# Kernel tuning notes

Hardware: AMD Instinct MI355X
Metric: run time of the kernel (lower is better)

## Reference

```python
import jax, jax.numpy as jnp
import numpy as np

C = 256; G = 16; GC = C // G; K = 3; P = K * K
N = 4; H = 64; W = 64
PAD = 1; OFFSET_SCALE = 1.0; LN_EPS = 1e-5


def setup_inputs() -> dict:
    key = jax.random.key(0)
    ks = jax.random.split(key, 8)
    s = 0.02
    return {
        "x": jax.random.normal(ks[0], (N, C, H, W), jnp.float32),
        "dw_w": jax.random.normal(ks[1], (C, 1, K, K), jnp.float32) * s,
        "dw_b": jnp.zeros((C,), jnp.float32),
        "ln_g": jnp.ones((C,), jnp.float32),
        "ln_b": jnp.zeros((C,), jnp.float32),
        "off_w": jax.random.normal(ks[2], (C, G * P * 2), jnp.float32) * s,
        "off_b": jnp.zeros((G * P * 2,), jnp.float32),
        "mask_w": jax.random.normal(ks[3], (C, G * P), jnp.float32) * s,
        "mask_b": jnp.zeros((G * P,), jnp.float32),
        "inp_w": jax.random.normal(ks[4], (C, C), jnp.float32) * s,
        "inp_b": jnp.zeros((C,), jnp.float32),
        "out_w": jax.random.normal(ks[5], (C, C), jnp.float32) * s,
        "out_b": jnp.zeros((C,), jnp.float32),
    }


def _dcnv3_nchw(x, dw_w, dw_b, ln_g, ln_b, off_w, off_b, mask_w, mask_b,
                inp_w, inp_b, out_w, out_b):
    # NCHW -> NHWC (wrapper permute)
    xn = jnp.transpose(x, (0, 2, 3, 1))                      # (N,H,W,C)
    x_proj = xn @ inp_w + inp_b                              # input_proj

    # offset/mask branch: depthwise conv (NCHW) -> LayerNorm (channels-last) -> GELU
    x1 = jax.lax.conv_general_dilated(
        x, dw_w, window_strides=(1, 1), padding=((PAD, PAD), (PAD, PAD)),
        dimension_numbers=("NCHW", "OIHW", "NCHW"), feature_group_count=C)
    x1 = jnp.transpose(x1, (0, 2, 3, 1)) + dw_b
    mu = x1.mean(-1, keepdims=True)
    var = ((x1 - mu) ** 2).mean(-1, keepdims=True)
    x1 = (x1 - mu) * jax.lax.rsqrt(var + LN_EPS) * ln_g + ln_b
    x1 = jax.nn.gelu(x1, approximate=False)

    offset = (x1 @ off_w + off_b).reshape(N, H, W, G, P, 2)  # (x,y) pairs
    mask = jax.nn.softmax((x1 @ mask_w + mask_b).reshape(N, H, W, G, P), axis=-1)

    # pad sampled feature map with zeros (F.pad before sampling)
    xp = jnp.pad(x_proj, ((0, 0), (PAD, PAD), (PAD, PAD), (0, 0)))
    Hin, Win = H + 2 * PAD, W + 2 * PAD
    xg = xp.reshape(N, Hin, Win, G, GC)

    # reference points, normalized by padded size
    ref_y = (jnp.arange(H, dtype=jnp.float32) + PAD + 0.5) / Hin
    ref_x = (jnp.arange(W, dtype=jnp.float32) + PAD + 0.5) / Win
    ref = jnp.stack([jnp.broadcast_to(ref_x[None, :], (H, W)),
                     jnp.broadcast_to(ref_y[:, None], (H, W))], -1)  # (H,W,2)

    # dilation grid: x varies in the outer loop (torch meshgrid 'ij')
    d = jnp.arange(K, dtype=jnp.float32) - (K - 1) // 2     # [-1,0,1]
    gx = jnp.repeat(d, K) / Win
    gy = jnp.tile(d, K) / Hin
    grid = jnp.stack([gx, gy], -1)                           # (P,2)

    norm = jnp.array([Win, Hin], jnp.float32)
    loc = (ref[None, :, :, None, None, :] + grid * OFFSET_SCALE
           + offset * OFFSET_SCALE / norm)                   # (N,H,W,G,P,2)

    # grid_sample bilinear, align_corners=False, zero padding
    px = loc[..., 0] * Win - 0.5
    py = loc[..., 1] * Hin - 0.5
    x0 = jnp.floor(px); y0 = jnp.floor(py)
    wx = px - x0; wy = py - y0
    x0i = x0.astype(jnp.int32); y0i = y0.astype(jnp.int32)

    n_idx = jnp.arange(N)[:, None, None, None, None]
    g_idx = jnp.arange(G)[None, None, None, :, None]

    def corner(iy, ix, w):
        valid = (iy >= 0) & (iy < Hin) & (ix >= 0) & (ix < Win)
        v = xg[n_idx, jnp.clip(iy, 0, Hin - 1), jnp.clip(ix, 0, Win - 1), g_idx]
        wgt = jnp.where(valid, w, 0.0) * mask                # fold mask into weights
        return jnp.einsum("nhwgp,nhwgpc->nhwgc", wgt, v)

    out = (corner(y0i, x0i, (1 - wy) * (1 - wx))
           + corner(y0i, x0i + 1, (1 - wy) * wx)
           + corner(y0i + 1, x0i, wy * (1 - wx))
           + corner(y0i + 1, x0i + 1, wy * wx))               # (N,H,W,G,GC)

    out = out.reshape(N, H, W, C) @ out_w + out_b            # output_proj
    return jnp.transpose(out, (0, 3, 1, 2))                  # NHWC -> NCHW


def reference(x, dw_w, dw_b, ln_g, ln_b, off_w, off_b, mask_w, mask_b,
              inp_w, inp_b, out_w, out_b):
    return _dcnv3_nchw(x, dw_w, dw_b, ln_g, ln_b, off_w, off_b,
                       mask_w, mask_b, inp_w, inp_b, out_w, out_b)
```

## Files before the change

### kernel.cpp

```cpp
#include <hip/hip_runtime.h>
#include <hip/hip_bf16.h>
#include <math.h>


using bf16x8 = __attribute__((ext_vector_type(8))) short;
using f32x4  = __attribute__((ext_vector_type(4))) float;

#define GLOBAL_AS __attribute__((address_space(1)))
#define LDS_AS    __attribute__((address_space(3)))

static __device__ inline void g2lds16(const void* g, void* l) {
  __builtin_amdgcn_global_load_lds((const GLOBAL_AS int*)g, (LDS_AS int*)l, 16, 0, 0);
}
static __device__ inline unsigned short f2bf(float v) {
  __hip_bfloat16 b = __float2bfloat16(v);
  return *reinterpret_cast<unsigned short*>(&b);
}
static __device__ inline float us2f(unsigned short u) {
  union { unsigned u; float f; } c; c.u = ((unsigned)u) << 16; return c.f;
}

__global__ __launch_bounds__(256) void prep_w_k(
    const float* __restrict__ inp_w, const float* __restrict__ off_w,
    const float* __restrict__ off_b, const float* __restrict__ mask_w,
    const float* __restrict__ mask_b, const float* __restrict__ out_w,
    __hip_bfloat16* __restrict__ BtI, __hip_bfloat16* __restrict__ BtOM,
    __hip_bfloat16* __restrict__ BtO, float* __restrict__ bOM)
{
  const int b = blockIdx.x, t = threadIdx.x;
  if (b < 256) {
    int n = b;
    BtI[n * 256 + t] = __float2bfloat16(inp_w[t * 256 + n]);
  } else if (b < 768) {
    int n = b - 256;
    float v = 0.f;
    if (n < 288) v = off_w[t * 288 + n];
    else if (n < 432) v = mask_w[t * 144 + (n - 288)];
    BtOM[n * 256 + t] = __float2bfloat16(v);
    if (b == 256) {
      for (int idx = t; idx < 512; idx += 256) {
        float bv = (idx < 288) ? off_b[idx] : ((idx < 432) ? mask_b[idx - 288] : 0.f);
        bOM[idx] = bv;
      }
    }
  } else {
    int n = b - 768;
    BtO[n * 256 + t] = __float2bfloat16(out_w[t * 256 + n]);
  }
}

__global__ __launch_bounds__(1024) void stage2_gi_k(
    const float* __restrict__ x,
    const float* __restrict__ dw_w, const float* __restrict__ dw_b,
    const float* __restrict__ ln_g, const float* __restrict__ ln_b,
    const __hip_bfloat16* __restrict__ BtOM, const float* __restrict__ bOM,
    __hip_bfloat16* __restrict__ om,
    const __hip_bfloat16* __restrict__ BtI, const float* __restrict__ inp_b,
    __hip_bfloat16* __restrict__ xpu)
{
  __shared__ __align__(16) char smem[57344];
  const int bid = blockIdx.x;
  const int t = threadIdx.x;

  if (bid >= 256) {
    unsigned short* A = (unsigned short*)smem;
    float* ftile = (float*)(smem + 33792);

    const int strip = bid - 256;
    const int n4 = strip >> 6, hw0 = (strip & 63) * 64;
    const float* xb = x + (size_t)n4 * 1048576 + hw0;

    const int cl0 = t >> 6, wl0 = t & 63;
    const int cl1 = (t + 1024) >> 6, wl1 = (t + 1024) & 63;
    float p0 = xb[(size_t)cl0 * 4096 + wl0];
    float p1 = xb[(size_t)cl1 * 4096 + wl1];

    for (int ck = 0; ck < 8; ++ck) {
      const int ch0 = ck * 32;
      ftile[cl0 * 65 + wl0] = p0;
      ftile[cl1 * 65 + wl1] = p1;
      if (ck < 7) {
        p0 = xb[(size_t)(ch0 + 32 + cl0) * 4096 + wl0];
        p1 = xb[(size_t)(ch0 + 32 + cl1) * 4096 + wl1];
      }
      __syncthreads();
      {
        int px = t >> 4, cq2 = t & 15;
        unsigned short b0 = f2bf(ftile[(cq2 * 2) * 65 + px]);
        unsigned short b1 = f2bf(ftile[(cq2 * 2 + 1) * 65 + px]);
        *(unsigned*)&A[px * 264 + ch0 + cq2 * 2] =
            (unsigned)b0 | ((unsigned)b1 << 16);
      }
      __syncthreads();
    }

    const int wave = t >> 6, lane = t & 63;
    const int quad = lane >> 4, lr = lane & 15;
    const int wm = wave >> 2, wn = wave & 3;

    bf16x8 areg[8];
    #pragma unroll
    for (int s = 0; s < 8; ++s)
      areg[s] = *(const bf16x8*)&A[(wm * 16 + lr) * 264 + s * 32 + quad * 8];
    __syncthreads();

    auto stageI = [&](int s, int buf) {
      int col = t >> 2, kq = t & 3;
      g2lds16(BtI + (size_t)col * 256 + s * 32 + kq * 8,
              smem + buf * 16384 + t * 16);
    };

    f32x4 acc[4];
    #pragma unroll
    for (int i = 0; i < 4; ++i) acc[i] = (f32x4){0.f, 0.f, 0.f, 0.f};

    stageI(0, 0);
    __syncthreads();
    #pragma unroll
    for (int s = 0; s < 8; ++s) {
      if (s < 7) stageI(s + 1, (s + 1) & 1);
      const short* B = (const short*)(smem + (s & 1) * 16384);
      bf16x8 bfr[4];
      #pragma unroll
      for (int ni = 0; ni < 4; ++ni)
        bfr[ni] = *(const bf16x8*)&B[(wn * 64 + ni * 16 + lr) * 32 + quad * 8];
      #pragma unroll
      for (int ni = 0; ni < 4; ++ni)
        acc[ni] = __builtin_amdgcn_mfma_f32_16x16x32_bf16(areg[s], bfr[ni], acc[ni], 0, 0, 0);
      __syncthreads();
    }

    const size_t m0 = (size_t)strip * 64;
    #pragma unroll
    for (int ni = 0; ni < 4; ++ni) {
      int col = wn * 64 + ni * 16 + lr;
      float bv = inp_b[col];
      #pragma unroll
      for (int reg = 0; reg < 4; ++reg) {
        size_t m = m0 + wm * 16 + quad * 4 + reg;
        xpu[m * 256 + col] = __float2bfloat16(acc[ni][reg] + bv);
      }
    }
    return;
  }

  unsigned short* x1t = (unsigned short*)smem;
  float* psq  = (float*)(smem + 33792);
  float* murs = (float*)(smem + 41984);

  const int blk = ((bid & 7) << 5) | (bid >> 3);
  const int n4 = blk >> 6, h = blk & 63;
  const int w = t & 63, q = t >> 6;

  const float* xb = x + (size_t)n4 * 1048576;
  const bool hm = (h > 0), hp = (h < 63);
  float av[16];
  float s1 = 0.f, s2 = 0.f;

  #pragma unroll 2
  for (int j = 0; j < 8; ++j) {
    #pragma unroll
    for (int u = 0; u < 2; ++u) {
      const int c = q * 16 + 2 * j + u;
      const float* xc = xb + (size_t)c * 4096 + h * 64 + w;
      float v0 = hm ? xc[-64] : 0.f;
      float v1 = xc[0];
      float v2 = hp ? xc[64] : 0.f;
      const float* wp = dw_w + c * 9;
      float a = dw_b[c];
      #pragma unroll
      for (int dh = 0; dh < 3; ++dh) {
        float v = (dh == 0) ? v0 : (dh == 1) ? v1 : v2;
        float vm = __shfl(v, w - 1, 64);
        float vp = __shfl(v, w + 1, 64);
        if (w == 0)  vm = 0.f;
        if (w == 63) vp = 0.f;
        a = fmaf(vm, wp[dh * 3 + 0], a);
        a = fmaf(v,  wp[dh * 3 + 1], a);
        a = fmaf(vp, wp[dh * 3 + 2], a);
      }
      s1 += a;
      s2 = fmaf(a, a, s2);
      av[2 * j + u] = a;
    }
  }

  psq[q * 64 + w] = s1;
  psq[1024 + q * 64 + w] = s2;
  __syncthreads();
  if (t < 64) {
    float a = 0.f, b = 0.f;
    #pragma unroll
    for (int j = 0; j < 16; ++j) { a += psq[j * 64 + t]; b += psq[1024 + j * 64 + t]; }
    float mu = a * (1.f / 256.f);
    murs[t] = mu;
    murs[64 + t] = rsqrtf(b * (1.f / 256.f) - mu * mu + 1e-5f);
  }
  __syncthreads();
  {
    float mu = murs[w], rs = murs[64 + w];
    #pragma unroll
    for (int j = 0; j < 8; ++j) {
      int c = q * 16 + 2 * j;
      float y0 = fmaf((av[2 * j] - mu) * rs, ln_g[c], ln_b[c]);
      float y1 = fmaf((av[2 * j + 1] - mu) * rs, ln_g[c + 1], ln_b[c + 1]);
      float g0 = 0.5f * y0 * (1.f + erff(y0 * 0.70710678f));
      float g1 = 0.5f * y1 * (1.f + erff(y1 * 0.70710678f));
      *(unsigned*)&x1t[w * 264 + c] = (unsigned)f2bf(g0) | ((unsigned)f2bf(g1) << 16);
    }
  }
  __syncthreads();

  const int wave = t >> 6, lane = t & 63;
  const int quad = lane >> 4, lr = lane & 15;
  const int wm = wave >> 2, wn = wave & 3;

  bf16x8 areg[8];
  #pragma unroll
  for (int s = 0; s < 8; ++s)
    areg[s] = *(const bf16x8*)&x1t[(wm * 16 + lr) * 264 + s * 32 + quad * 8];
  __syncthreads();

  auto stageOM = [&](int s, int buf) {
    char* dst = smem + buf * 28672;
    int col = t >> 2, kq = t & 3;
    g2lds16(BtOM + (size_t)col * 256 + s * 32 + kq * 8, dst + t * 16);
    int jj = t + 1024;
    if (jj < 1792) {
      int col2 = jj >> 2, kq2 = jj & 3;
      g2lds16(BtOM + (size_t)col2 * 256 + s * 32 + kq2 * 8, dst + jj * 16);
    }
  };

  f32x4 acc[7];
  #pragma unroll
  for (int i = 0; i < 7; ++i) acc[i] = (f32x4){0.f, 0.f, 0.f, 0.f};

  stageOM(0, 0);
  __syncthreads();
  #pragma unroll
  for (int s = 0; s < 8; ++s) {
    if (s < 7) stageOM(s + 1, (s + 1) & 1);
    const short* B = (const short*)(smem + (s & 1) * 28672);
    bf16x8 bfr[7];
    #pragma unroll
    for (int ni = 0; ni < 7; ++ni)
      bfr[ni] = *(const bf16x8*)&B[(wn * 112 + ni * 16 + lr) * 32 + quad * 8];
    #pragma unroll
    for (int ni = 0; ni < 7; ++ni)
      acc[ni] = __builtin_amdgcn_mfma_f32_16x16x32_bf16(areg[s], bfr[ni], acc[ni], 0, 0, 0);
    __syncthreads();
  }

  const size_t pix0 = (size_t)n4 * 4096 + (size_t)h * 64;
  #pragma unroll
  for (int ni = 0; ni < 7; ++ni) {
    int col = wn * 112 + ni * 16 + lr;
    if (col < 432) {
      float bv = bOM[col];
      #pragma unroll
      for (int reg = 0; reg < 4; ++reg) {
        int m = wm * 16 + quad * 4 + reg;
        om[(pix0 + m) * 448 + col] = __float2bfloat16(acc[ni][reg] + bv);
      }
    }
  }
}

__global__ __launch_bounds__(512) void fused_so_k(
    const __hip_bfloat16* __restrict__ xpu, const __hip_bfloat16* __restrict__ om,
    const __hip_bfloat16* __restrict__ BtO, const float* __restrict__ out_b,
    float* __restrict__ out)
{
  __shared__ __align__(16) char smem[49664];
  unsigned short* st = (unsigned short*)smem;

  const int bid = blockIdx.x;
  const int swz = ((bid & 7) << 6) | (bid >> 3);
  const int pix0 = swz << 5;
  const int t = threadIdx.x;

  auto stageO = [&](int s, int buf) {
    char* dst = smem + 16896 + buf * 16384;
    #pragma unroll
    for (int r = 0; r < 2; ++r) {
      int j = t + r * 512;
      int col = j >> 2, kq = j & 3;
      g2lds16(BtO + (size_t)col * 256 + s * 32 + kq * 8, dst + j * 16);
    }
  };

  stageO(0, 0);

  {
    const int pl = t >> 4, g = t & 15;
    const int pix = pix0 + pl;
    const int n4s = pix >> 12;
    const int hw = pix & 4095;
    const int h = hw >> 6, w = hw & 63;
    const unsigned short* omp = (const unsigned short*)om + (size_t)pix * 448;

    float mk[9];
    {
      float mx = -1e30f;
      #pragma unroll
      for (int p = 0; p < 9; ++p) { mk[p] = us2f(omp[288 + g * 9 + p]); mx = fmaxf(mx, mk[p]); }
      float se = 0.f;
      #pragma unroll
      for (int p = 0; p < 9; ++p) { mk[p] = __expf(mk[p] - mx); se += mk[p]; }
      float inv = 1.f / se;
      #pragma unroll
      for (int p = 0; p < 9; ++p) mk[p] *= inv;
    }

    const __hip_bfloat16* xpg = xpu + (g << 4);
    float ax[16];
    #pragma unroll
    for (int i = 0; i < 16; ++i) ax[i] = 0.f;

    auto corner = [&](int iy, int ix, float wt) {
      if ((unsigned)(iy - 1) >= 64u || (unsigned)(ix - 1) >= 64u) return;
      const __hip_bfloat16* src =
          xpg + ((size_t)((n4s << 12) + (iy - 1) * 64 + (ix - 1)) << 8);
      uint4 u0 = *(const uint4*)src;
      uint4 u1 = *(const uint4*)(src + 8);
      const unsigned uu[8] = {u0.x, u0.y, u0.z, u0.w, u1.x, u1.y, u1.z, u1.w};
      #pragma unroll
      for (int i = 0; i < 8; ++i) {
        float lo = us2f((unsigned short)(uu[i] & 0xffff));
        float hi = us2f((unsigned short)(uu[i] >> 16));
        ax[2 * i + 0] = fmaf(wt, lo, ax[2 * i + 0]);
        ax[2 * i + 1] = fmaf(wt, hi, ax[2 * i + 1]);
      }
    };

    #pragma unroll
    for (int p = 0; p < 9; ++p) {
      float ox = us2f(omp[g * 18 + 2 * p]), oy = us2f(omp[g * 18 + 2 * p + 1]);
      float px = (float)(w + p / 3) + ox;
      float py = (float)(h + p % 3) + oy;
      float xf = floorf(px), yf = floorf(py);
      float wx = px - xf, wy = py - yf;
      int ix = (int)xf, iy = (int)yf;
      float m = mk[p];
      corner(iy,     ix,     (1.f - wy) * (1.f - wx) * m);
      corner(iy,     ix + 1, (1.f - wy) * wx * m);
      corner(iy + 1, ix,     wy * (1.f - wx) * m);
      corner(iy + 1, ix + 1, wy * wx * m);
    }

    unsigned short ub[16];
    #pragma unroll
    for (int i = 0; i < 16; ++i) ub[i] = f2bf(ax[i]);
    uint4 u0, u1;
    u0.x = (unsigned)ub[0] | ((unsigned)ub[1] << 16);
    u0.y = (unsigned)ub[2] | ((unsigned)ub[3] << 16);
    u0.z = (unsigned)ub[4] | ((unsigned)ub[5] << 16);
    u0.w = (unsigned)ub[6] | ((unsigned)ub[7] << 16);
    u1.x = (unsigned)ub[8] | ((unsigned)ub[9] << 16);
    u1.y = (unsigned)ub[10] | ((unsigned)ub[11] << 16);
    u1.z = (unsigned)ub[12] | ((unsigned)ub[13] << 16);
    u1.w = (unsigned)ub[14] | ((unsigned)ub[15] << 16);
    *(uint4*)&st[pl * 264 + g * 16] = u0;
    *(uint4*)&st[pl * 264 + g * 16 + 8] = u1;
  }
  __syncthreads();

  const int wave = t >> 6, lane = t & 63;
  const int quad = lane >> 4, lr = lane & 15;
  const int wm = wave >> 2, wn = wave & 3;

  bf16x8 areg[8];
  #pragma unroll
  for (int s = 0; s < 8; ++s)
    areg[s] = *(const bf16x8*)&st[(wm * 16 + lr) * 264 + s * 32 + quad * 8];

  f32x4 acc[4];
  #pragma unroll
  for (int i = 0; i < 4; ++i) acc[i] = (f32x4){0.f, 0.f, 0.f, 0.f};

  #pragma unroll
  for (int s = 0; s < 8; ++s) {
    if (s < 7) stageO(s + 1, (s + 1) & 1);
    const short* B = (const short*)(smem + 16896 + (s & 1) * 16384);
    bf16x8 bfr[4];
    #pragma unroll
    for (int ni = 0; ni < 4; ++ni)
      bfr[ni] = *(const bf16x8*)&B[(wn * 64 + ni * 16 + lr) * 32 + quad * 8];
    #pragma unroll
    for (int ni = 0; ni < 4; ++ni)
      acc[ni] = __builtin_amdgcn_mfma_f32_16x16x32_bf16(areg[s], bfr[ni], acc[ni], 0, 0, 0);
    __syncthreads();
  }

  const int n4 = pix0 >> 12, hw0 = pix0 & 4095;
  #pragma unroll
  for (int ni = 0; ni < 4; ++ni) {
    int col = wn * 64 + ni * 16 + lr;
    float bv = out_b[col];
    float4 v;
    v.x = acc[ni][0] + bv; v.y = acc[ni][1] + bv;
    v.z = acc[ni][2] + bv; v.w = acc[ni][3] + bv;
    *(float4*)&out[(size_t)(n4 * 256 + col) * 4096 + hw0 + wm * 16 + quad * 4] = v;
  }
}

extern "C" void kernel_launch(void* const* d_in, const int* in_sizes, int n_in,
                              void* d_out, int out_size, void* d_ws, size_t ws_size,
                              hipStream_t stream) {
  const float* x      = (const float*)d_in[0];
  const float* dw_w   = (const float*)d_in[1];
  const float* dw_b   = (const float*)d_in[2];
  const float* ln_g   = (const float*)d_in[3];
  const float* ln_b   = (const float*)d_in[4];
  const float* off_w  = (const float*)d_in[5];
  const float* off_b  = (const float*)d_in[6];
  const float* mask_w = (const float*)d_in[7];
  const float* mask_b = (const float*)d_in[8];
  const float* inp_w  = (const float*)d_in[9];
  const float* inp_b  = (const float*)d_in[10];
  const float* out_w  = (const float*)d_in[11];
  const float* out_b  = (const float*)d_in[12];
  float* out = (float*)d_out;

  char* w0 = (char*)d_ws;
  __hip_bfloat16* xpu  = (__hip_bfloat16*)(w0);
  __hip_bfloat16* om   = (__hip_bfloat16*)(w0 + 8388608);
  __hip_bfloat16* BtI  = (__hip_bfloat16*)(w0 + 23068672);
  __hip_bfloat16* BtOM = (__hip_bfloat16*)(w0 + 23199744);
  __hip_bfloat16* BtO  = (__hip_bfloat16*)(w0 + 23461888);
  float*          bOM  = (float*)(w0 + 23592960);
  if (ws_size < 23595008) return;

  prep_w_k<<<1024, 256, 0, stream>>>(inp_w, off_w, off_b, mask_w, mask_b,
                                     out_w, BtI, BtOM, BtO, bOM);
  stage2_gi_k<<<512, 1024, 0, stream>>>(x, dw_w, dw_b, ln_g, ln_b, BtOM, bOM,
                                        om, BtI, inp_b, xpu);
  fused_so_k<<<512, 512, 0, stream>>>(xpu, om, BtO, out_b, out);
}
```

Baseline: 152.2 us.

## Move offset/mask GEMM into sampling kernel, keep results in LDS

The offset/mask projection GEMM moves out of the depthwise/LayerNorm kernel, which now writes the GELU activations (256 bf16 per pixel) to global memory. The sampling kernel loads those activations, runs the 448-column GEMM per 32-pixel tile, and keeps the offsets and mask logits in LDS instead of reading them back from global. This drops the 448-wide om buffer round trip and shortens the first kernel, at the cost of more LDS per block (about 78 KB, which may reduce occupancy) and a longer sampling kernel.

```diff
diff --git a/kernel.cpp b/kernel.cpp
--- a/kernel.cpp
+++ b/kernel.cpp
@@ -53,12 +53,10 @@
     const float* __restrict__ x,
     const float* __restrict__ dw_w, const float* __restrict__ dw_b,
     const float* __restrict__ ln_g, const float* __restrict__ ln_b,
-    const __hip_bfloat16* __restrict__ BtOM, const float* __restrict__ bOM,
-    __hip_bfloat16* __restrict__ om,
     const __hip_bfloat16* __restrict__ BtI, const float* __restrict__ inp_b,
-    __hip_bfloat16* __restrict__ xpu)
+    __hip_bfloat16* __restrict__ xpu, __hip_bfloat16* __restrict__ x1g)
 {
-  __shared__ __align__(16) char smem[57344];
+  __shared__ __align__(16) char smem[42496];
   const int bid = blockIdx.x;
   const int t = threadIdx.x;
 
@@ -211,77 +209,51 @@
   }
   __syncthreads();
 
-  const int wave = t >> 6, lane = t & 63;
-  const int quad = lane >> 4, lr = lane & 15;
-  const int wm = wave >> 2, wn = wave & 3;
-
-  bf16x8 areg[8];
-  #pragma unroll
-  for (int s = 0; s < 8; ++s)
-    areg[s] = *(const bf16x8*)&x1t[(wm * 16 + lr) * 264 + s * 32 + quad * 8];
-  __syncthreads();
-
-  auto stageOM = [&](int s, int buf) {
-    char* dst = smem + buf * 28672;
-    int col = t >> 2, kq = t & 3;
-    g2lds16(BtOM + (size_t)col * 256 + s * 32 + kq * 8, dst + t * 16);
-    int jj = t + 1024;
-    if (jj < 1792) {
-      int col2 = jj >> 2, kq2 = jj & 3;
-      g2lds16(BtOM + (size_t)col2 * 256 + s * 32 + kq2 * 8, dst + jj * 16);
-    }
-  };
-
-  f32x4 acc[7];
-  #pragma unroll
-  for (int i = 0; i < 7; ++i) acc[i] = (f32x4){0.f, 0.f, 0.f, 0.f};
-
-  stageOM(0, 0);
-  __syncthreads();
-  #pragma unroll
-  for (int s = 0; s < 8; ++s) {
-    if (s < 7) stageOM(s + 1, (s + 1) & 1);
-    const short* B = (const short*)(smem + (s & 1) * 28672);
-    bf16x8 bfr[7];
-    #pragma unroll
-    for (int ni = 0; ni < 7; ++ni)
-      bfr[ni] = *(const bf16x8*)&B[(wn * 112 + ni * 16 + lr) * 32 + quad * 8];
-    #pragma unroll
-    for (int ni = 0; ni < 7; ++ni)
-      acc[ni] = __builtin_amdgcn_mfma_f32_16x16x32_bf16(areg[s], bfr[ni], acc[ni], 0, 0, 0);
-    __syncthreads();
-  }
-
   const size_t pix0 = (size_t)n4 * 4096 + (size_t)h * 64;
   #pragma unroll
-  for (int ni = 0; ni < 7; ++ni) {
-    int col = wn * 112 + ni * 16 + lr;
-    if (col < 432) {
-      float bv = bOM[col];
-      #pragma unroll
-      for (int reg = 0; reg < 4; ++reg) {
-        int m = wm * 16 + quad * 4 + reg;
-        om[(pix0 + m) * 448 + col] = __float2bfloat16(acc[ni][reg] + bv);
-      }
-    }
+  for (int r = 0; r < 2; ++r) {
+    int j = t + r * 1024;
+    int px = j >> 5, cu = j & 31;
+    *(uint4*)&x1g[(pix0 + px) * 256 + cu * 8] = *(const uint4*)&x1t[px * 264 + cu * 8];
   }
 }
 
 __global__ __launch_bounds__(512) void fused_so_k(
-    const __hip_bfloat16* __restrict__ xpu, const __hip_bfloat16* __restrict__ om,
+    const __hip_bfloat16* __restrict__ x1g, const __hip_bfloat16* __restrict__ xpu,
+    const __hip_bfloat16* __restrict__ BtOM, const float* __restrict__ bOM,
     const __hip_bfloat16* __restrict__ BtO, const float* __restrict__ out_b,
     float* __restrict__ out)
 {
-  __shared__ __align__(16) char smem[49664];
-  unsigned short* st = (unsigned short*)smem;
+  __shared__ __align__(16) char smem[78336];
+  unsigned short* x1s = (unsigned short*)smem;
+  unsigned short* st  = (unsigned short*)smem;
+  unsigned short* Som = (unsigned short*)(smem + 16896);
 
   const int bid = blockIdx.x;
   const int swz = ((bid & 7) << 6) | (bid >> 3);
   const int pix0 = swz << 5;
   const int t = threadIdx.x;
 
+  const int wave = t >> 6, lane = t & 63;
+  const int quad = lane >> 4, lr = lane & 15;
+  const int wm = wave >> 2, wn = wave & 3;
+
+  auto stageB = [&](int s, int buf) {
+    char* dst = smem + 16896 + buf * 28672;
+    #pragma unroll
+    for (int r = 0; r < 3; ++r) {
+      int j = t + r * 512;
+      int col = j >> 2, kq = j & 3;
+      g2lds16(BtOM + (size_t)col * 256 + s * 32 + kq * 8, dst + j * 16);
+    }
+    if (t < 256) {
+      int j = t + 1536;
+      int col = j >> 2, kq = j & 3;
+      g2lds16(BtOM + (size_t)col * 256 + s * 32 + kq * 8, dst + j * 16);
+    }
+  };
   auto stageO = [&](int s, int buf) {
-    char* dst = smem + 16896 + buf * 16384;
+    char* dst = smem + 45568 + buf * 16384;
     #pragma unroll
     for (int r = 0; r < 2; ++r) {
       int j = t + r * 512;
@@ -289,6 +261,50 @@
       g2lds16(BtO + (size_t)col * 256 + s * 32 + kq * 8, dst + j * 16);
     }
   };
+
+  #pragma unroll
+  for (int r = 0; r < 2; ++r) {
+    int j = t + r * 512;
+    int px = j >> 5, cu = j & 31;
+    g2lds16(x1g + (size_t)(pix0 + px) * 256 + cu * 8, smem + j * 16);
+  }
+  stageB(0, 0);
+  __syncthreads();
+
+  bf16x8 areg[8];
+  #pragma unroll
+  for (int s = 0; s < 8; ++s)
+    areg[s] = *(const bf16x8*)&x1s[(wm * 16 + lr) * 256 + s * 32 + quad * 8];
+
+  f32x4 acc[7];
+  #pragma unroll
+  for (int i = 0; i < 7; ++i) acc[i] = (f32x4){0.f, 0.f, 0.f, 0.f};
+
+  #pragma unroll
+  for (int s = 0; s < 8; ++s) {
+    if (s < 7) stageB(s + 1, (s + 1) & 1);
+    const short* B = (const short*)(smem + 16896 + (s & 1) * 28672);
+    bf16x8 bfr[7];
+    #pragma unroll
+    for (int ni = 0; ni < 7; ++ni)
+      bfr[ni] = *(const bf16x8*)&B[(wn * 112 + ni * 16 + lr) * 32 + quad * 8];
+    #pragma unroll
+    for (int ni = 0; ni < 7; ++ni)
+      acc[ni] = __builtin_amdgcn_mfma_f32_16x16x32_bf16(areg[s], bfr[ni], acc[ni], 0, 0, 0);
+    __syncthreads();
+  }
+
+  #pragma unroll
+  for (int ni = 0; ni < 7; ++ni) {
+    int col = wn * 112 + ni * 16 + lr;
+    float bv = bOM[col];
+    #pragma unroll
+    for (int reg = 0; reg < 4; ++reg) {
+      int m = wm * 16 + quad * 4 + reg;
+      Som[m * 448 + col] = f2bf(acc[ni][reg] + bv);
+    }
+  }
+  __syncthreads();
 
   stageO(0, 0);
 
@@ -298,7 +314,7 @@
     const int n4s = pix >> 12;
     const int hw = pix & 4095;
     const int h = hw >> 6, w = hw & 63;
-    const unsigned short* omp = (const unsigned short*)om + (size_t)pix * 448;
+    const unsigned short* omp = Som + pl * 448;
 
     float mk[9];
     {
@@ -366,30 +382,26 @@
   }
   __syncthreads();
 
-  const int wave = t >> 6, lane = t & 63;
-  const int quad = lane >> 4, lr = lane & 15;
-  const int wm = wave >> 2, wn = wave & 3;
-
-  bf16x8 areg[8];
+  bf16x8 areg2[8];
   #pragma unroll
   for (int s = 0; s < 8; ++s)
-    areg[s] = *(const bf16x8*)&st[(wm * 16 + lr) * 264 + s * 32 + quad * 8];
-
-  f32x4 acc[4];
-  #pragma unroll
-  for (int i = 0; i < 4; ++i) acc[i] = (f32x4){0.f, 0.f, 0.f, 0.f};
+    areg2[s] = *(const bf16x8*)&st[(wm * 16 + lr) * 264 + s * 32 + quad * 8];
+
+  f32x4 acc2[4];
+  #pragma unroll
+  for (int i = 0; i < 4; ++i) acc2[i] = (f32x4){0.f, 0.f, 0.f, 0.f};
 
   #pragma unroll
   for (int s = 0; s < 8; ++s) {
     if (s < 7) stageO(s + 1, (s + 1) & 1);
-    const short* B = (const short*)(smem + 16896 + (s & 1) * 16384);
+    const short* B = (const short*)(smem + 45568 + (s & 1) * 16384);
     bf16x8 bfr[4];
     #pragma unroll
     for (int ni = 0; ni < 4; ++ni)
       bfr[ni] = *(const bf16x8*)&B[(wn * 64 + ni * 16 + lr) * 32 + quad * 8];
     #pragma unroll
     for (int ni = 0; ni < 4; ++ni)
-      acc[ni] = __builtin_amdgcn_mfma_f32_16x16x32_bf16(areg[s], bfr[ni], acc[ni], 0, 0, 0);
+      acc2[ni] = __builtin_amdgcn_mfma_f32_16x16x32_bf16(areg2[s], bfr[ni], acc2[ni], 0, 0, 0);
     __syncthreads();
   }
 
@@ -399,8 +411,8 @@
     int col = wn * 64 + ni * 16 + lr;
     float bv = out_b[col];
     float4 v;
-    v.x = acc[ni][0] + bv; v.y = acc[ni][1] + bv;
-    v.z = acc[ni][2] + bv; v.w = acc[ni][3] + bv;
+    v.x = acc2[ni][0] + bv; v.y = acc2[ni][1] + bv;
+    v.z = acc2[ni][2] + bv; v.w = acc2[ni][3] + bv;
     *(float4*)&out[(size_t)(n4 * 256 + col) * 4096 + hw0 + wm * 16 + quad * 4] = v;
   }
 }
@@ -425,16 +437,16 @@
 
   char* w0 = (char*)d_ws;
   __hip_bfloat16* xpu  = (__hip_bfloat16*)(w0);
-  __hip_bfloat16* om   = (__hip_bfloat16*)(w0 + 8388608);
-  __hip_bfloat16* BtI  = (__hip_bfloat16*)(w0 + 23068672);
-  __hip_bfloat16* BtOM = (__hip_bfloat16*)(w0 + 23199744);
-  __hip_bfloat16* BtO  = (__hip_bfloat16*)(w0 + 23461888);
-  float*          bOM  = (float*)(w0 + 23592960);
-  if (ws_size < 23595008) return;
+  __hip_bfloat16* x1g  = (__hip_bfloat16*)(w0 + 8388608);
+  __hip_bfloat16* BtI  = (__hip_bfloat16*)(w0 + 16777216);
+  __hip_bfloat16* BtOM = (__hip_bfloat16*)(w0 + 16908288);
+  __hip_bfloat16* BtO  = (__hip_bfloat16*)(w0 + 17170432);
+  float*          bOM  = (float*)(w0 + 17301504);
+  if (ws_size < 17303552) return;
 
   prep_w_k<<<1024, 256, 0, stream>>>(inp_w, off_w, off_b, mask_w, mask_b,
                                      out_w, BtI, BtOM, BtO, bOM);
-  stage2_gi_k<<<512, 1024, 0, stream>>>(x, dw_w, dw_b, ln_g, ln_b, BtOM, bOM,
-                                        om, BtI, inp_b, xpu);
-  fused_so_k<<<512, 512, 0, stream>>>(xpu, om, BtO, out_b, out);
-}
+  stage2_gi_k<<<512, 1024, 0, stream>>>(x, dw_w, dw_b, ln_g, ln_b,
+                                        BtI, inp_b, xpu, x1g);
+  fused_so_k<<<512, 512, 0, stream>>>(x1g, xpu, BtOM, bOM, BtO, out_b, out);
+}
```

After: 147.0 us. 3.4% less time.
